# Kernel optimization log

Measured on AMD Instinct MI355X. Metric: run time of the kernel, lower is better.

Reference implementation:

```python
import jax, jax.numpy as jnp
import numpy as np

N = 500_000
E = 16_000_000
H = 128
EPS_COS = 1e-6
EPS_NORM = 1e-12


def _inf_normalize(x):
    # torch F.normalize(p=inf, dim=0): divide each column by max-abs over nodes
    m = jnp.max(jnp.abs(x), axis=0, keepdims=True)
    return x / jnp.maximum(m, EPS_NORM)


def _sage_mean(x, src, dst, n):
    # mean over incoming edges: hn_aggr[v] = mean_{(u->v)} x[u]; 0 if no in-edges (DGL convention)
    msg = x[src]                                   # [E, F] gather
    s = jax.ops.segment_sum(msg, dst, num_segments=n)
    cnt = jax.ops.segment_sum(jnp.ones((dst.shape[0], 1), x.dtype), dst, num_segments=n)
    return jnp.where(cnt > 0, s / jnp.maximum(cnt, 1.0), 0.0)


def setup_inputs() -> dict:
    key = jax.random.key(0)
    ks = jax.random.split(key, 20)
    inp = {
        "hop": jax.random.uniform(ks[0], (N, 1), jnp.float32),
        "remaining_distance": jax.random.uniform(ks[1], (N, 1), jnp.float32),
        "expected_travel_time": jax.random.uniform(ks[2], (N, 1), jnp.float32),
        "current_time": jax.random.uniform(ks[3], (N, 1), jnp.float32) * 1440.0,
        "curr2neigh": jax.random.normal(ks[4], (N, 3), jnp.float32),
        "curr2target": jax.random.normal(ks[5], (N, 3), jnp.float32),
        "nid": jnp.arange(N, dtype=jnp.int32),
        "src": jax.random.randint(ks[6], (E,), 0, N, jnp.int32),
        "dst": jax.random.randint(ks[7], (E,), 0, N, jnp.int32),
        "curr_node": 0,
        "aW2": jax.random.normal(ks[8], (5, H), jnp.float32) * 0.3,
        "ab2": jax.random.normal(ks[9], (H,), jnp.float32) * 0.1,
        "aW3": jax.random.normal(ks[10], (H, H // 2), jnp.float32) * 0.1,
        "ab3": jax.random.normal(ks[11], (H // 2,), jnp.float32) * 0.1,
        "aW4": jax.random.normal(ks[12], (H // 2, 1), jnp.float32) * 0.1,
        "ab4": jax.random.normal(ks[13], (1,), jnp.float32) * 0.1,
        "cW2": jax.random.normal(ks[14], (6, H), jnp.float32) * 0.3,
        "cb2": jax.random.normal(ks[15], (H,), jnp.float32) * 0.1,
        "cW3": jax.random.normal(ks[16], (H, H // 2), jnp.float32) * 0.1,
        "cb3": jax.random.normal(ks[17], (H // 2,), jnp.float32) * 0.1,
        "cW4": jax.random.normal(ks[18], (H // 2, 1), jnp.float32) * 0.1,
        "cb4": jax.random.normal(ks[19], (1,), jnp.float32) * 0.1,
    }
    return inp


def reference(hop, remaining_distance, expected_travel_time, current_time,
              curr2neigh, curr2target, nid, src, dst, curr_node,
              aW2, ab2, aW3, ab3, aW4, ab4,
              cW2, cb2, cW3, cb3, cW4, cb4):
    n = hop.shape[0]
    # ---- actor ----
    dot = jnp.sum(curr2neigh * curr2target, axis=1)
    na = jnp.maximum(jnp.linalg.norm(curr2neigh, axis=1), EPS_COS)
    nb = jnp.maximum(jnp.linalg.norm(curr2target, axis=1), EPS_COS)
    cos_sim = (dot / (na * nb))[:, None]           # [N,1]
    feat = jnp.concatenate([hop, cos_sim, remaining_distance, expected_travel_time], axis=1)
    feat = _inf_normalize(feat)
    feat = jnp.concatenate([current_time / 1440.0, feat], axis=1)  # [N,5]
    x = _sage_mean(feat, src, dst, n)              # [N,5]
    concat_x = (feat + x) * 0.5
    x = jax.nn.sigmoid(concat_x @ aW2 + ab2)       # [N,H]
    x = jax.nn.sigmoid(x @ aW3 + ab3)              # [N,H/2]
    policy = (x @ aW4 + ab4)[:, 0]                 # [N]
    policy = jnp.where(nid == curr_node, -jnp.inf, policy)
    policy_mask = jax.nn.softmax(policy, axis=-1)  # N >= 9 so no padding branch
    # ---- critic ----
    featc = jnp.concatenate([hop, remaining_distance], axis=1)
    featc = _inf_normalize(featc)
    featc = jnp.concatenate([current_time / 1440.0, featc], axis=1)  # [N,3]
    x1 = _sage_mean(featc, src, dst, n)            # [N,3]
    avg0 = jnp.mean(featc, axis=0)                 # dgl.mean_nodes, single graph
    avg1 = jnp.mean(x1, axis=0)
    cx = jnp.concatenate([avg0, avg1])[None, :]    # [1,6]
    v = jax.nn.sigmoid(cx @ cW2 + cb2)
    v = jax.nn.sigmoid(v @ cW3 + cb3)
    value = (v @ cW4 + cb4).squeeze()
    return (policy_mask, value)
```

## Files before the change

kernel.cpp:

```cpp
#include <hip/hip_runtime.h>
#include <hip/hip_bf16.h>


typedef unsigned int u32;
typedef unsigned long long u64;
typedef long long i64t;
typedef __attribute__((ext_vector_type(4))) float f32x4;

#define BP_STRIDE 16
#define CHUNK 8192

__device__ __forceinline__ float sigf(float x) { return 1.0f / (1.0f + __expf(-x)); }

__device__ __forceinline__ float waveReduceSum(float v) {
#pragma unroll
    for (int off = 32; off > 0; off >>= 1) v += __shfl_down(v, off, 64);
    return v;
}
__device__ __forceinline__ float waveReduceMax(float v) {
#pragma unroll
    for (int off = 32; off > 0; off >>= 1) v = fmaxf(v, __shfl_down(v, off, 64));
    return v;
}


__global__ __launch_bounds__(256) void k1_prep(
    const float* __restrict__ hop, const float* __restrict__ rd,
    const float* __restrict__ ett, const float* __restrict__ ct,
    const float* __restrict__ c2n, const float* __restrict__ c2t,
    float4* __restrict__ featA, u64* __restrict__ packed,
    float* __restrict__ partials, int n)
{
    int i = blockIdx.x * blockDim.x + threadIdx.x;
    float ah = 0.f, ac = 0.f, ar = 0.f, ae = 0.f, sc = 0.f, sh = 0.f, sr = 0.f;
    if (i < n) {
        float h = hop[i], r = rd[i], e = ett[i], c = ct[i];
        float ax = c2n[3*i+0], ay = c2n[3*i+1], az = c2n[3*i+2];
        float bx = c2t[3*i+0], by = c2t[3*i+1], bz = c2t[3*i+2];
        float dot = ax*bx + ay*by + az*bz;
        float na = fmaxf(sqrtf(ax*ax + ay*ay + az*az), 1e-6f);
        float nb = fmaxf(sqrtf(bx*bx + by*by + bz*bz), 1e-6f);
        float cs = dot / (na * nb);
        featA[i] = make_float4(h, cs, r, e);

        u64 qc = (u64)(u32)rintf(c * (16.0f/1440.0f));
        u64 qh = (u64)(u32)rintf(h * 16.0f);
        u64 qs = (u64)(u32)rintf((cs + 1.0f) * 16.0f);
        u64 qr = (u64)(u32)rintf(r * 16.0f);
        u64 qe = (u64)(u32)rintf(e * 16.0f);
        packed[i] = qc | (qh << 11) | (qs << 22) | (qr << 34) | (qe << 45) | (1ULL << 56);

        ah = fabsf(h); ac = fabsf(cs); ar = fabsf(r); ae = fabsf(e);
        sc = c; sh = h; sr = r;
    }
    ah = waveReduceMax(ah); ac = waveReduceMax(ac);
    ar = waveReduceMax(ar); ae = waveReduceMax(ae);
    sc = waveReduceSum(sc); sh = waveReduceSum(sh); sr = waveReduceSum(sr);

    __shared__ float red[4][7];
    int wid = threadIdx.x >> 6;
    if ((threadIdx.x & 63) == 0) {
        red[wid][0] = ah; red[wid][1] = ac; red[wid][2] = ar; red[wid][3] = ae;
        red[wid][4] = sc; red[wid][5] = sh; red[wid][6] = sr;
    }
    __syncthreads();
    if (threadIdx.x == 0) {
        float* p = partials + (size_t)blockIdx.x * 8;
        p[0] = fmaxf(fmaxf(red[0][0], red[1][0]), fmaxf(red[2][0], red[3][0]));
        p[1] = fmaxf(fmaxf(red[0][1], red[1][1]), fmaxf(red[2][1], red[3][1]));
        p[2] = fmaxf(fmaxf(red[0][2], red[1][2]), fmaxf(red[2][2], red[3][2]));
        p[3] = fmaxf(fmaxf(red[0][3], red[1][3]), fmaxf(red[2][3], red[3][3]));
        p[4] = red[0][4] + red[1][4] + red[2][4] + red[3][4];
        p[5] = red[0][5] + red[1][5] + red[2][5] + red[3][5];
        p[6] = red[0][6] + red[1][6] + red[2][6] + red[3][6];
    }
}

__global__ __launch_bounds__(256) void k1b_reduce(
    const float* __restrict__ partials, float* __restrict__ accum, int nblocks)
{
    float mh = 0.f, mc = 0.f, mr = 0.f, me = 0.f, sc = 0.f, sh = 0.f, sr = 0.f;
    for (int b = threadIdx.x; b < nblocks; b += 256) {
        const float* p = partials + (size_t)b * 8;
        mh = fmaxf(mh, p[0]); mc = fmaxf(mc, p[1]);
        mr = fmaxf(mr, p[2]); me = fmaxf(me, p[3]);
        sc += p[4]; sh += p[5]; sr += p[6];
    }
    mh = waveReduceMax(mh); mc = waveReduceMax(mc);
    mr = waveReduceMax(mr); me = waveReduceMax(me);
    sc = waveReduceSum(sc); sh = waveReduceSum(sh); sr = waveReduceSum(sr);
    __shared__ float red[4][7];
    int wid = threadIdx.x >> 6;
    if ((threadIdx.x & 63) == 0) {
        red[wid][0] = mh; red[wid][1] = mc; red[wid][2] = mr; red[wid][3] = me;
        red[wid][4] = sc; red[wid][5] = sh; red[wid][6] = sr;
    }
    __syncthreads();
    if (threadIdx.x == 0) {
        accum[0] = fmaxf(fmaxf(red[0][0], red[1][0]), fmaxf(red[2][0], red[3][0]));
        accum[1] = fmaxf(fmaxf(red[0][1], red[1][1]), fmaxf(red[2][1], red[3][1]));
        accum[2] = fmaxf(fmaxf(red[0][2], red[1][2]), fmaxf(red[2][2], red[3][2]));
        accum[3] = fmaxf(fmaxf(red[0][3], red[1][3]), fmaxf(red[2][3], red[3][3]));
        accum[4] = red[0][4] + red[1][4] + red[2][4] + red[3][4];
        accum[5] = red[0][5] + red[1][5] + red[2][5] + red[3][5];
        accum[6] = red[0][6] + red[1][6] + red[2][6] + red[3][6];
    }
}

__global__ __launch_bounds__(256) void k2a_sort(
    const int* __restrict__ src, const int* __restrict__ dst,
    u32* __restrict__ records, u32* __restrict__ bucketPos,
    int E, int nb, int cap)
{
    __shared__ u32 hist[128];
    __shared__ u32 hoff[128];
    __shared__ u32 lstart[128];
    __shared__ u32 gbase[128];
    __shared__ u32 sorted[CHUNK];
    __shared__ unsigned char bkt[CHUNK];

    int tid = threadIdx.x;
    int e0 = blockIdx.x * CHUNK;
    int cnt = min(CHUNK, E - e0);
    if (cnt <= 0) return;
    int cnt4 = cnt >> 2;
    const int4* dst4 = (const int4*)(dst + e0);
    const int4* src4 = (const int4*)(src + e0);

    for (int i = tid; i < nb; i += 256) { hist[i] = 0; hoff[i] = 0; }
    __syncthreads();

    for (int i = tid; i < cnt4; i += 256) {
        int4 d = dst4[i];
        atomicAdd(&hist[d.x >> 12], 1u);
        atomicAdd(&hist[d.y >> 12], 1u);
        atomicAdd(&hist[d.z >> 12], 1u);
        atomicAdd(&hist[d.w >> 12], 1u);
    }
    for (int i = (cnt4 << 2) + tid; i < cnt; i += 256)
        atomicAdd(&hist[dst[e0 + i] >> 12], 1u);
    __syncthreads();

    if (tid == 0) {
        u32 run = 0;
        for (int b = 0; b < nb; ++b) { lstart[b] = run; run += hist[b]; }
    }
    __syncthreads();
    for (int b = tid; b < nb; b += 256)
        gbase[b] = atomicAdd(&bucketPos[b * BP_STRIDE], hist[b]);
    __syncthreads();

    for (int i = tid; i < cnt4; i += 256) {
        int4 d = dst4[i];
        int4 s = src4[i];
        {
            u32 b = (u32)d.x >> 12;
            u32 ls = lstart[b] + atomicAdd(&hoff[b], 1u);
            sorted[ls] = ((u32)s.x << 12) | ((u32)d.x & 4095u);
            bkt[ls] = (unsigned char)b;
        }
        {
            u32 b = (u32)d.y >> 12;
            u32 ls = lstart[b] + atomicAdd(&hoff[b], 1u);
            sorted[ls] = ((u32)s.y << 12) | ((u32)d.y & 4095u);
            bkt[ls] = (unsigned char)b;
        }
        {
            u32 b = (u32)d.z >> 12;
            u32 ls = lstart[b] + atomicAdd(&hoff[b], 1u);
            sorted[ls] = ((u32)s.z << 12) | ((u32)d.z & 4095u);
            bkt[ls] = (unsigned char)b;
        }
        {
            u32 b = (u32)d.w >> 12;
            u32 ls = lstart[b] + atomicAdd(&hoff[b], 1u);
            sorted[ls] = ((u32)s.w << 12) | ((u32)d.w & 4095u);
            bkt[ls] = (unsigned char)b;
        }
    }
    for (int i = (cnt4 << 2) + tid; i < cnt; i += 256) {
        int d = dst[e0 + i];
        u32 b = (u32)d >> 12;
        u32 ls = lstart[b] + atomicAdd(&hoff[b], 1u);
        sorted[ls] = ((u32)src[e0 + i] << 12) | ((u32)d & 4095u);
        bkt[ls] = (unsigned char)b;
    }
    __syncthreads();

    for (int i = tid; i < cnt; i += 256) {
        u32 b = bkt[i];
        u32 pos = gbase[b] + ((u32)i - lstart[b]);
        if (pos < (u32)cap)
            records[(size_t)b * cap + pos] = sorted[i];
    }
}

__global__ __launch_bounds__(256) void k2b_accum(
    const u32* __restrict__ records, const u32* __restrict__ bucketPos,
    const u64* __restrict__ packed, u64* __restrict__ S2rep,
    int n, int cap, int nsl)
{
    __shared__ u64 acc[4096];
    int bucket = blockIdx.x / nsl;
    int slice  = blockIdx.x % nsl;
    int nodeBase = bucket << 12;
    int nNodes = min(4096, n - nodeBase);
    for (int i = threadIdx.x; i < 4096; i += 256) acc[i] = 0;
    __syncthreads();
    u32 cnt = bucketPos[bucket * BP_STRIDE];
    if (cnt > (u32)cap) cnt = (u32)cap;
    u32 lo = (u32)(((u64)cnt * (u32)slice) / (u32)nsl);
    u32 hi = (u32)(((u64)cnt * (u32)(slice + 1)) / (u32)nsl);
    const u32* rec = records + (size_t)bucket * cap;
    u32 r = lo + threadIdx.x;
    for (; r + 768 < hi; r += 1024) {
        u32 v0 = rec[r];
        u32 v1 = rec[r + 256];
        u32 v2 = rec[r + 512];
        u32 v3 = rec[r + 768];
        u64 p0 = packed[v0 >> 12];
        u64 p1 = packed[v1 >> 12];
        u64 p2 = packed[v2 >> 12];
        u64 p3 = packed[v3 >> 12];
        atomicAdd(&acc[v0 & 4095u], p0);
        atomicAdd(&acc[v1 & 4095u], p1);
        atomicAdd(&acc[v2 & 4095u], p2);
        atomicAdd(&acc[v3 & 4095u], p3);
    }
    for (; r < hi; r += 256) {
        u32 v = rec[r];
        atomicAdd(&acc[v & 4095u], packed[v >> 12]);
    }
    __syncthreads();
    u64* dstp = S2rep + (size_t)slice * n + nodeBase;
    for (int i = threadIdx.x; i < nNodes; i += 256) dstp[i] = acc[i];
}

__global__ __launch_bounds__(256, 4) void k3_mlp(
    const float4* __restrict__ featA, const float* __restrict__ ct,
    const u64* __restrict__ S2rep, int nsl, const int* __restrict__ nid,
    const int* __restrict__ currp,
    const float* __restrict__ aW2, const float* __restrict__ ab2,
    const float* __restrict__ aW3, const float* __restrict__ ab3,
    const float* __restrict__ aW4, const float* __restrict__ ab4,
    const float* __restrict__ accum, float* __restrict__ partials2,
    float* __restrict__ out, int n)
{
    __shared__ char w3t8[8192];
    __shared__ char hb8[32768];

    int tid  = threadIdx.x;
    int lane = tid & 63;
    int wid  = tid >> 6;
    int lc   = lane & 15;
    int lg   = lane >> 4;

    for (int t = tid; t < 2048; t += 256) {
        int col = t & 63;
        int j0  = (t >> 6) << 2;
        float w0 = aW3[(j0 + 0) * 64 + col];
        float w1 = aW3[(j0 + 1) * 64 + col];
        float w2 = aW3[(j0 + 2) * 64 + col];
        float w3 = aW3[(j0 + 3) * 64 + col];
        u32 pk = (u32)__builtin_amdgcn_cvt_pk_fp8_f32(w0, w1, 0, false);
        pk = (u32)__builtin_amdgcn_cvt_pk_fp8_f32(w2, w3, (int)pk, true);
        *(u32*)(w3t8 + col * 128 + (j0 ^ ((col & 7) << 4))) = pk;
    }

    int i0 = blockIdx.x * 256 + tid;
    int i = i0 < n ? i0 : n - 1;
    bool valid = i0 < n;

    float inv_mh = 1.0f / fmaxf(accum[0], 1e-12f);
    float inv_mc = 1.0f / fmaxf(accum[1], 1e-12f);
    float inv_mr = 1.0f / fmaxf(accum[2], 1e-12f);
    float inv_me = 1.0f / fmaxf(accum[3], 1e-12f);
    int curr = currp[0];

    float4 f = featA[i];
    float c = ct[i];
    u64 P = 0;
    for (int s = 0; s < nsl; ++s) P += S2rep[(size_t)s * n + i];
    u32 qct = (u32)(P         & 0x7FFULL);
    u32 qh  = (u32)((P >> 11) & 0x7FFULL);
    u32 qcs = (u32)((P >> 22) & 0xFFFULL);
    u32 qr  = (u32)((P >> 34) & 0x7FFULL);
    u32 qe  = (u32)((P >> 45) & 0x7FFULL);
    u32 deg = (u32)(P >> 56);
    float icd = deg ? 1.0f / (16.0f * (float)deg) : 0.f;
    float x0 = (float)qct * icd;
    float x1 = (float)qh  * icd * inv_mh;
    float x2 = deg ? ((float)qcs * icd - 1.0f) * inv_mc : 0.f;
    float x3 = (float)qr  * icd * inv_mr;
    float x4 = (float)qe  * icd * inv_me;
    float f0 = c * (1.0f/1440.0f);
    float f1 = f.x * inv_mh, f2 = f.y * inv_mc, f3 = f.z * inv_mr, f4 = f.w * inv_me;
    float g0 = 0.5f*(f0+x0), g1 = 0.5f*(f1+x1), g2 = 0.5f*(f2+x2),
          g3 = 0.5f*(f3+x3), g4 = 0.5f*(f4+x4);

    {
        int rowbase = tid * 128;
        int swz = (tid & 7) << 4;
        for (int j = 0; j < 128; j += 16) {
            float hv[16];
#pragma unroll
            for (int jj = 0; jj < 16; ++jj) {
                float t = ab2[j + jj];
                t = fmaf(g0, aW2[j + jj],       t);
                t = fmaf(g1, aW2[128 + j + jj], t);
                t = fmaf(g2, aW2[256 + j + jj], t);
                t = fmaf(g3, aW2[384 + j + jj], t);
                t = fmaf(g4, aW2[512 + j + jj], t);
                float e = __expf(-t);
                hv[jj] = __builtin_amdgcn_rcpf(1.0f + e);
            }
            int4 w;
            u32 a;
            a = (u32)__builtin_amdgcn_cvt_pk_fp8_f32(hv[0],  hv[1],  0, false);
            a = (u32)__builtin_amdgcn_cvt_pk_fp8_f32(hv[2],  hv[3],  (int)a, true);
            w.x = (int)a;
            a = (u32)__builtin_amdgcn_cvt_pk_fp8_f32(hv[4],  hv[5],  0, false);
            a = (u32)__builtin_amdgcn_cvt_pk_fp8_f32(hv[6],  hv[7],  (int)a, true);
            w.y = (int)a;
            a = (u32)__builtin_amdgcn_cvt_pk_fp8_f32(hv[8],  hv[9],  0, false);
            a = (u32)__builtin_amdgcn_cvt_pk_fp8_f32(hv[10], hv[11], (int)a, true);
            w.z = (int)a;
            a = (u32)__builtin_amdgcn_cvt_pk_fp8_f32(hv[12], hv[13], 0, false);
            a = (u32)__builtin_amdgcn_cvt_pk_fp8_f32(hv[14], hv[15], (int)a, true);
            w.w = (int)a;
            *(int4*)(hb8 + rowbase + (j ^ swz)) = w;
        }
    }
    __syncthreads();

    i64t bfr[4][4];
#pragma unroll
    for (int nt = 0; nt < 4; ++nt) {
#pragma unroll
        for (int kc = 0; kc < 4; ++kc) {
            int col = nt * 16 + lc;
            int boff = col * 128 + ((kc * 32 + lg * 8) ^ ((col & 7) << 4));
            bfr[nt][kc] = *(const i64t*)(w3t8 + boff);
        }
    }
    float b3v[4], w4v[4];
#pragma unroll
    for (int nt = 0; nt < 4; ++nt) {
        b3v[nt] = ab3[nt * 16 + lc];
        w4v[nt] = aW4[nt * 16 + lc];
    }
    float bias4 = ab4[0];

    int waveSlot = wid * 64;
    float evloc = 0.f;
#pragma unroll
    for (int mt = 0; mt < 4; ++mt) {
        i64t afr[4];
#pragma unroll
        for (int kc = 0; kc < 4; ++kc) {
            int row = waveSlot + mt * 16 + lc;
            int aoff = row * 128 + ((kc * 32 + lg * 8) ^ ((row & 7) << 4));
            afr[kc] = *(const i64t*)(hb8 + aoff);
        }
        float ps0 = 0.f, ps1 = 0.f, ps2 = 0.f, ps3 = 0.f;
#pragma unroll
        for (int nt = 0; nt < 4; ++nt) {
            f32x4 d = {0.f, 0.f, 0.f, 0.f};
            d = __builtin_amdgcn_mfma_f32_16x16x32_fp8_fp8(afr[0], bfr[nt][0], d, 0, 0, 0);
            d = __builtin_amdgcn_mfma_f32_16x16x32_fp8_fp8(afr[1], bfr[nt][1], d, 0, 0, 0);
            d = __builtin_amdgcn_mfma_f32_16x16x32_fp8_fp8(afr[2], bfr[nt][2], d, 0, 0, 0);
            d = __builtin_amdgcn_mfma_f32_16x16x32_fp8_fp8(afr[3], bfr[nt][3], d, 0, 0, 0);
            float b3 = b3v[nt], w4 = w4v[nt];
            ps0 = fmaf(sigf(d[0] + b3), w4, ps0);
            ps1 = fmaf(sigf(d[1] + b3), w4, ps1);
            ps2 = fmaf(sigf(d[2] + b3), w4, ps2);
            ps3 = fmaf(sigf(d[3] + b3), w4, ps3);
        }
#pragma unroll
        for (int off = 1; off < 16; off <<= 1) {
            ps0 += __shfl_xor(ps0, off, 64);
            ps1 += __shfl_xor(ps1, off, 64);
            ps2 += __shfl_xor(ps2, off, 64);
            ps3 += __shfl_xor(ps3, off, 64);
        }
        if (lc < 4) {
            float pv = (lc == 0) ? ps0 : (lc == 1) ? ps1 : (lc == 2) ? ps2 : ps3;
            pv += bias4;
            int slot = waveSlot + mt * 16 + lg * 4 + lc;
            int gi = blockIdx.x * 256 + slot;
            if (gi < n) {
                float evv = (nid[gi] == curr) ? 0.f : __expf(pv);
                out[gi] = evv;
                evloc += evv;
            }
        }
    }

    float r0s = valid ? x0 : 0.f;
    float r1s = valid ? x1 : 0.f;
    float r3s = valid ? x3 : 0.f;

    float ev = waveReduceSum(evloc);
    r0s = waveReduceSum(r0s);
    r1s = waveReduceSum(r1s);
    r3s = waveReduceSum(r3s);

    __syncthreads();
    float (*red)[4] = (float(*)[4])hb8;
    if ((tid & 63) == 0) {
        red[wid][0] = ev; red[wid][1] = r0s; red[wid][2] = r1s; red[wid][3] = r3s;
    }
    __syncthreads();
    if (tid == 0) {
        float* p2 = partials2 + (size_t)blockIdx.x * 4;
        p2[0] = red[0][0] + red[1][0] + red[2][0] + red[3][0];
        p2[1] = red[0][1] + red[1][1] + red[2][1] + red[3][1];
        p2[2] = red[0][2] + red[1][2] + red[2][2] + red[3][2];
        p2[3] = red[0][3] + red[1][3] + red[2][3] + red[3][3];
    }
}

__global__ __launch_bounds__(256) void k3b_reduce(
    const float* __restrict__ partials2, float* __restrict__ accum, int nblocks)
{
    float s0 = 0.f, s1 = 0.f, s2 = 0.f, s3 = 0.f;
    for (int b = threadIdx.x; b < nblocks; b += 256) {
        const float* p = partials2 + (size_t)b * 4;
        s0 += p[0]; s1 += p[1]; s2 += p[2]; s3 += p[3];
    }
    s0 = waveReduceSum(s0); s1 = waveReduceSum(s1);
    s2 = waveReduceSum(s2); s3 = waveReduceSum(s3);
    __shared__ float red[4][4];
    int wid = threadIdx.x >> 6;
    if ((threadIdx.x & 63) == 0) {
        red[wid][0] = s0; red[wid][1] = s1; red[wid][2] = s2; red[wid][3] = s3;
    }
    __syncthreads();
    if (threadIdx.x == 0) {
        accum[7]  = red[0][0] + red[1][0] + red[2][0] + red[3][0];
        accum[8]  = red[0][1] + red[1][1] + red[2][1] + red[3][1];
        accum[9]  = red[0][2] + red[1][2] + red[2][2] + red[3][2];
        accum[10] = red[0][3] + red[1][3] + red[2][3] + red[3][3];
    }
}

__global__ void k4_critic(const float* __restrict__ accum,
                          const float* __restrict__ cW2, const float* __restrict__ cb2,
                          const float* __restrict__ cW3, const float* __restrict__ cb3,
                          const float* __restrict__ cW4, const float* __restrict__ cb4,
                          float* __restrict__ out, int n)
{
    __shared__ float v1[128];
    __shared__ float v2[64];
    int t = threadIdx.x;
    float invN = 1.0f / (float)n;
    float inv_mh = 1.0f / fmaxf(accum[0], 1e-12f);
    float inv_mr = 1.0f / fmaxf(accum[2], 1e-12f);
    float cx0 = accum[4] * invN * (1.0f / 1440.0f);
    float cx1 = accum[5] * invN * inv_mh;
    float cx2 = accum[6] * invN * inv_mr;
    float cx3 = accum[8] * invN;
    float cx4 = accum[9] * invN;
    float cx5 = accum[10] * invN;
    if (t < 128) {
        float a = cb2[t];
        a = fmaf(cx0, cW2[t],       a);
        a = fmaf(cx1, cW2[128 + t], a);
        a = fmaf(cx2, cW2[256 + t], a);
        a = fmaf(cx3, cW2[384 + t], a);
        a = fmaf(cx4, cW2[512 + t], a);
        a = fmaf(cx5, cW2[640 + t], a);
        v1[t] = sigf(a);
    }
    __syncthreads();
    if (t < 64) {
        float a = cb3[t];
        for (int j = 0; j < 128; ++j) a = fmaf(v1[j], cW3[j * 64 + t], a);
        v2[t] = sigf(a);
    }
    __syncthreads();
    if (t == 0) {
        float a = cb4[0];
        for (int k = 0; k < 64; ++k) a = fmaf(v2[k], cW4[k], a);
        out[n] = a;
    }
}

__global__ void k5_scale(float* __restrict__ out, const float* __restrict__ accum, int n)
{
    int i = blockIdx.x * blockDim.x + threadIdx.x;
    float inv = 1.0f / accum[7];
    if (i < n) out[i] *= inv;
}

__global__ void k2_atomic(const int* __restrict__ src, const int* __restrict__ dst,
                          const u64* __restrict__ packed, u64* __restrict__ S2, int E)
{
    int stride = gridDim.x * blockDim.x;
    for (int e = blockIdx.x * blockDim.x + threadIdx.x; e < E; e += stride) {
        atomicAdd(S2 + dst[e], packed[src[e]]);
    }
}

extern "C" void kernel_launch(void* const* d_in, const int* in_sizes, int n_in,
                              void* d_out, int out_size, void* d_ws, size_t ws_size,
                              hipStream_t stream)
{
    const float* hop = (const float*)d_in[0];
    const float* rd  = (const float*)d_in[1];
    const float* ett = (const float*)d_in[2];
    const float* ct  = (const float*)d_in[3];
    const float* c2n = (const float*)d_in[4];
    const float* c2t = (const float*)d_in[5];
    const int*   nid = (const int*)d_in[6];
    const int*   src = (const int*)d_in[7];
    const int*   dst = (const int*)d_in[8];
    const int*   cur = (const int*)d_in[9];
    const float* aW2 = (const float*)d_in[10];
    const float* ab2 = (const float*)d_in[11];
    const float* aW3 = (const float*)d_in[12];
    const float* ab3 = (const float*)d_in[13];
    const float* aW4 = (const float*)d_in[14];
    const float* ab4 = (const float*)d_in[15];
    const float* cW2 = (const float*)d_in[16];
    const float* cb2 = (const float*)d_in[17];
    const float* cW3 = (const float*)d_in[18];
    const float* cb3 = (const float*)d_in[19];
    const float* cW4 = (const float*)d_in[20];
    const float* cb4 = (const float*)d_in[21];

    int n = in_sizes[0];
    int E = in_sizes[7];
    float* out = (float*)d_out;

    const int NSL = 4;
    int nb  = (n + 4095) >> 12;
    int cap = E / (nb > 0 ? nb : 1) + 8192;
    int nbk = (n + 255) / 256;

    char* ws = (char*)d_ws;
    float4* featA  = (float4*)ws;
    u64*    packed = (u64*)(ws + (size_t)16 * n);
    u64*    S2rep  = (u64*)(ws + (size_t)24 * n);

    size_t tail_bucket = (size_t)56 * n;
    size_t tail_fb     = (size_t)32 * n;
    size_t tailsz = 256 + 8192 + (size_t)48 * nbk;
    size_t needed = tail_bucket + tailsz + (size_t)nb * cap * 4;
    bool bucketPath = (ws_size >= needed) && (nb <= 128);

    char* base = ws + (bucketPath ? tail_bucket : tail_fb);
    float* accum     = (float*)base;
    u32*   bucketPos = (u32*)(base + 256);
    float* partials  = (float*)(base + 256 + 8192);
    float* partials2 = (float*)(base + 256 + 8192 + (size_t)32 * nbk);
    u32*   records   = (u32*)(base + tailsz);

    if (bucketPath) {
        hipMemsetAsync(bucketPos, 0, 8192, stream);
        k1_prep<<<nbk, 256, 0, stream>>>(hop, rd, ett, ct, c2n, c2t, featA, packed, partials, n);
        k1b_reduce<<<1, 256, 0, stream>>>(partials, accum, nbk);
        int nchunks = (E + CHUNK - 1) / CHUNK;
        k2a_sort<<<nchunks, 256, 0, stream>>>(src, dst, records, bucketPos, E, nb, cap);
        k2b_accum<<<nb * NSL, 256, 0, stream>>>(records, bucketPos, packed, S2rep, n, cap, NSL);
        k3_mlp<<<nbk, 256, 0, stream>>>(featA, ct, S2rep, NSL, nid, cur,
                                        aW2, ab2, aW3, ab3, aW4, ab4, accum, partials2, out, n);
        k3b_reduce<<<1, 256, 0, stream>>>(partials2, accum, nbk);
    } else {
        u64* S2f = (u64*)(ws + (size_t)24 * n);
        hipMemsetAsync(S2f, 0, (size_t)8 * n, stream);
        k1_prep<<<nbk, 256, 0, stream>>>(hop, rd, ett, ct, c2n, c2t, featA, packed, partials, n);
        k1b_reduce<<<1, 256, 0, stream>>>(partials, accum, nbk);
        k2_atomic<<<4096, 256, 0, stream>>>(src, dst, packed, S2f, E);
        k3_mlp<<<nbk, 256, 0, stream>>>(featA, ct, S2f, 1, nid, cur,
                                        aW2, ab2, aW3, ab3, aW4, ab4, accum, partials2, out, n);
        k3b_reduce<<<1, 256, 0, stream>>>(partials2, accum, nbk);
    }
    k4_critic<<<1, 128, 0, stream>>>(accum, cW2, cb2, cW3, cb3, cW4, cb4, out, n);
    k5_scale<<<nbk, 256, 0, stream>>>(out, accum, n);
}
```

Measured before the change: 253.4 us.

## Halve destination bucket size and derive bucket index by binary search

After: 283.1 us. +11.7%, slower.

```diff
diff --git a/kernel.cpp b/kernel.cpp
--- a/kernel.cpp
+++ b/kernel.cpp
@@ -9,6 +9,8 @@
 
 #define BP_STRIDE 16
 #define CHUNK 8192
+#define BSH 11
+#define BMASK 2047
 
 __device__ __forceinline__ float sigf(float x) { return 1.0f / (1.0f + __expf(-x)); }
 
@@ -112,12 +114,11 @@
     u32* __restrict__ records, u32* __restrict__ bucketPos,
     int E, int nb, int cap)
 {
-    __shared__ u32 hist[128];
-    __shared__ u32 hoff[128];
-    __shared__ u32 lstart[128];
-    __shared__ u32 gbase[128];
+    __shared__ u32 hist[256];
+    __shared__ u32 hoff[256];
+    __shared__ u32 lstart[260];
+    __shared__ u32 gbase[256];
     __shared__ u32 sorted[CHUNK];
-    __shared__ unsigned char bkt[CHUNK];
 
     int tid = threadIdx.x;
     int e0 = blockIdx.x * CHUNK;
@@ -132,18 +133,19 @@
 
     for (int i = tid; i < cnt4; i += 256) {
         int4 d = dst4[i];
-        atomicAdd(&hist[d.x >> 12], 1u);
-        atomicAdd(&hist[d.y >> 12], 1u);
-        atomicAdd(&hist[d.z >> 12], 1u);
-        atomicAdd(&hist[d.w >> 12], 1u);
+        atomicAdd(&hist[d.x >> BSH], 1u);
+        atomicAdd(&hist[d.y >> BSH], 1u);
+        atomicAdd(&hist[d.z >> BSH], 1u);
+        atomicAdd(&hist[d.w >> BSH], 1u);
     }
     for (int i = (cnt4 << 2) + tid; i < cnt; i += 256)
-        atomicAdd(&hist[dst[e0 + i] >> 12], 1u);
+        atomicAdd(&hist[dst[e0 + i] >> BSH], 1u);
     __syncthreads();
 
     if (tid == 0) {
         u32 run = 0;
         for (int b = 0; b < nb; ++b) { lstart[b] = run; run += hist[b]; }
+        lstart[nb] = run;
     }
     __syncthreads();
     for (int b = tid; b < nb; b += 256)
@@ -154,44 +156,45 @@
         int4 d = dst4[i];
         int4 s = src4[i];
         {
-            u32 b = (u32)d.x >> 12;
+            u32 b = (u32)d.x >> BSH;
             u32 ls = lstart[b] + atomicAdd(&hoff[b], 1u);
-            sorted[ls] = ((u32)s.x << 12) | ((u32)d.x & 4095u);
-            bkt[ls] = (unsigned char)b;
+            sorted[ls] = ((u32)s.x << BSH) | ((u32)d.x & BMASK);
         }
         {
-            u32 b = (u32)d.y >> 12;
+            u32 b = (u32)d.y >> BSH;
             u32 ls = lstart[b] + atomicAdd(&hoff[b], 1u);
-            sorted[ls] = ((u32)s.y << 12) | ((u32)d.y & 4095u);
-            bkt[ls] = (unsigned char)b;
+            sorted[ls] = ((u32)s.y << BSH) | ((u32)d.y & BMASK);
         }
         {
-            u32 b = (u32)d.z >> 12;
+            u32 b = (u32)d.z >> BSH;
             u32 ls = lstart[b] + atomicAdd(&hoff[b], 1u);
-            sorted[ls] = ((u32)s.z << 12) | ((u32)d.z & 4095u);
-            bkt[ls] = (unsigned char)b;
+            sorted[ls] = ((u32)s.z << BSH) | ((u32)d.z & BMASK);
         }
         {
-            u32 b = (u32)d.w >> 12;
+            u32 b = (u32)d.w >> BSH;
             u32 ls = lstart[b] + atomicAdd(&hoff[b], 1u);
-            sorted[ls] = ((u32)s.w << 12) | ((u32)d.w & 4095u);
-            bkt[ls] = (unsigned char)b;
+            sorted[ls] = ((u32)s.w << BSH) | ((u32)d.w & BMASK);
         }
     }
     for (int i = (cnt4 << 2) + tid; i < cnt; i += 256) {
         int d = dst[e0 + i];
-        u32 b = (u32)d >> 12;
+        u32 b = (u32)d >> BSH;
         u32 ls = lstart[b] + atomicAdd(&hoff[b], 1u);
-        sorted[ls] = ((u32)src[e0 + i] << 12) | ((u32)d & 4095u);
-        bkt[ls] = (unsigned char)b;
+        sorted[ls] = ((u32)src[e0 + i] << BSH) | ((u32)d & BMASK);
     }
     __syncthreads();
 
     for (int i = tid; i < cnt; i += 256) {
-        u32 b = bkt[i];
+        u32 rec = sorted[i];
+        int lo = 0, hi = nb;
+        while (hi - lo > 1) {
+            int mid = (lo + hi) >> 1;
+            if (lstart[mid] <= (u32)i) lo = mid; else hi = mid;
+        }
+        u32 b = (u32)lo;
         u32 pos = gbase[b] + ((u32)i - lstart[b]);
         if (pos < (u32)cap)
-            records[(size_t)b * cap + pos] = sorted[i];
+            records[(size_t)b * cap + pos] = rec;
     }
 }
 
@@ -200,12 +203,12 @@
     const u64* __restrict__ packed, u64* __restrict__ S2rep,
     int n, int cap, int nsl)
 {
-    __shared__ u64 acc[4096];
+    __shared__ u64 acc[2048];
     int bucket = blockIdx.x / nsl;
     int slice  = blockIdx.x % nsl;
-    int nodeBase = bucket << 12;
-    int nNodes = min(4096, n - nodeBase);
-    for (int i = threadIdx.x; i < 4096; i += 256) acc[i] = 0;
+    int nodeBase = bucket << BSH;
+    int nNodes = min(2048, n - nodeBase);
+    for (int i = threadIdx.x; i < 2048; i += 256) acc[i] = 0;
     __syncthreads();
     u32 cnt = bucketPos[bucket * BP_STRIDE];
     if (cnt > (u32)cap) cnt = (u32)cap;
@@ -218,18 +221,18 @@
         u32 v1 = rec[r + 256];
         u32 v2 = rec[r + 512];
         u32 v3 = rec[r + 768];
-        u64 p0 = packed[v0 >> 12];
-        u64 p1 = packed[v1 >> 12];
-        u64 p2 = packed[v2 >> 12];
-        u64 p3 = packed[v3 >> 12];
-        atomicAdd(&acc[v0 & 4095u], p0);
-        atomicAdd(&acc[v1 & 4095u], p1);
-        atomicAdd(&acc[v2 & 4095u], p2);
-        atomicAdd(&acc[v3 & 4095u], p3);
+        u64 p0 = packed[v0 >> BSH];
+        u64 p1 = packed[v1 >> BSH];
+        u64 p2 = packed[v2 >> BSH];
+        u64 p3 = packed[v3 >> BSH];
+        atomicAdd(&acc[v0 & BMASK], p0);
+        atomicAdd(&acc[v1 & BMASK], p1);
+        atomicAdd(&acc[v2 & BMASK], p2);
+        atomicAdd(&acc[v3 & BMASK], p3);
     }
     for (; r < hi; r += 256) {
         u32 v = rec[r];
-        atomicAdd(&acc[v & 4095u], packed[v >> 12]);
+        atomicAdd(&acc[v & BMASK], packed[v >> BSH]);
     }
     __syncthreads();
     u64* dstp = S2rep + (size_t)slice * n + nodeBase;
@@ -534,8 +537,8 @@
     float* out = (float*)d_out;
 
     const int NSL = 4;
-    int nb  = (n + 4095) >> 12;
-    int cap = E / (nb > 0 ? nb : 1) + 8192;
+    int nb  = (n + BMASK) >> BSH;
+    int cap = E / (nb > 0 ? nb : 1) + 4096;
     int nbk = (n + 255) / 256;
 
     char* ws = (char*)d_ws;
@@ -545,19 +548,19 @@
 
     size_t tail_bucket = (size_t)56 * n;
     size_t tail_fb     = (size_t)32 * n;
-    size_t tailsz = 256 + 8192 + (size_t)48 * nbk;
+    size_t tailsz = 256 + 16384 + (size_t)48 * nbk;
     size_t needed = tail_bucket + tailsz + (size_t)nb * cap * 4;
-    bool bucketPath = (ws_size >= needed) && (nb <= 128);
+    bool bucketPath = (ws_size >= needed) && (nb <= 256);
 
     char* base = ws + (bucketPath ? tail_bucket : tail_fb);
     float* accum     = (float*)base;
     u32*   bucketPos = (u32*)(base + 256);
-    float* partials  = (float*)(base + 256 + 8192);
-    float* partials2 = (float*)(base + 256 + 8192 + (size_t)32 * nbk);
+    float* partials  = (float*)(base + 256 + 16384);
+    float* partials2 = (float*)(base + 256 + 16384 + (size_t)32 * nbk);
     u32*   records   = (u32*)(base + tailsz);
 
     if (bucketPath) {
-        hipMemsetAsync(bucketPos, 0, 8192, stream);
+        hipMemsetAsync(bucketPos, 0, 16384, stream);
         k1_prep<<<nbk, 256, 0, stream>>>(hop, rd, ett, ct, c2n, c2t, featA, packed, partials, n);
         k1b_reduce<<<1, 256, 0, stream>>>(partials, accum, nbk);
         int nchunks = (E + CHUNK - 1) / CHUNK;
```
